# Kernel tuning notes

Hardware: AMD Instinct MI355X
Metric: run time of the kernel (lower is better)

The kernel has to match this reference:

```python
import jax, jax.numpy as jnp
import numpy as np

E, B, D, H, Z = 8, 16384, 512, 512, 64   # experts, batch, input_dim, hidden, latent
NHID = 2                                 # num_mlp_layers - 1 hidden-to-hidden layers


def setup_inputs() -> dict:
    key = jax.random.key(0)
    ks = jax.random.split(key, 12)

    def w(k, shape, fan_in):
        return (jax.random.normal(k, shape, jnp.float32) / np.sqrt(fan_in)).astype(jnp.float32)

    return {
        "x": jax.random.normal(ks[0], (B, D), jnp.float32),
        "eps": jax.random.normal(ks[1], (B, Z), jnp.float32),
        # stacked per-expert parameters (leading axis E)
        "enc_in_w": w(ks[2], (E, D, H), D), "enc_in_b": jnp.zeros((E, H), jnp.float32),
        "enc_hid_w": w(ks[3], (E, NHID, H, H), H), "enc_hid_b": jnp.zeros((E, NHID, H), jnp.float32),
        "mu_w": w(ks[4], (E, H, Z), H), "mu_b": jnp.zeros((E, Z), jnp.float32),
        "lv_w": w(ks[5], (E, H, Z), H), "lv_b": jnp.zeros((E, Z), jnp.float32),
        "dec_in_w": w(ks[6], (E, Z, H), Z), "dec_in_b": jnp.zeros((E, H), jnp.float32),
        "dec_hid_w": w(ks[7], (E, NHID, H, H), H), "dec_hid_b": jnp.zeros((E, NHID, H), jnp.float32),
        "dec_out_w": w(ks[8], (E, H, D), H), "dec_out_b": jnp.zeros((E, D), jnp.float32),
    }


def _moe_forward(x, eps, enc_in_w, enc_in_b, enc_hid_w, enc_hid_b,
                 mu_w, mu_b, lv_w, lv_b,
                 dec_in_w, dec_in_b, dec_hid_w, dec_hid_b, dec_out_w, dec_out_b):
    # ---- every expert tries the problem (dense, all experts over full batch) ----
    h = jax.nn.relu(jnp.einsum('bd,edh->ebh', x, enc_in_w) + enc_in_b[:, None, :])
    for i in range(NHID):
        h = jax.nn.relu(jnp.einsum('ebh,ehk->ebk', h, enc_hid_w[:, i]) + enc_hid_b[:, i, None, :])
    mu = jnp.einsum('ebh,ehz->ebz', h, mu_w) + mu_b[:, None, :]          # [E,B,Z]
    logvar = jnp.einsum('ebh,ehz->ebz', h, lv_w) + lv_b[:, None, :]       # [E,B,Z]
    z = mu + jnp.exp(0.5 * logvar) * eps[None, :, :]                      # reparameterize
    g = jax.nn.relu(jnp.einsum('ebz,ezh->ebh', z, dec_in_w) + dec_in_b[:, None, :])
    for i in range(NHID):
        g = jax.nn.relu(jnp.einsum('ebh,ehk->ebk', g, dec_hid_w[:, i]) + dec_hid_b[:, i, None, :])
    xhat = jnp.einsum('ebh,ehd->ebd', g, dec_out_w) + dec_out_b[:, None, :]  # [E,B,D]

    # ---- per-sample recon loss, pick best expert (torch.min over experts) ----
    recon = jnp.mean((xhat - x[None, :, :]) ** 2, axis=-1)                # [E,B]
    expert_idx = jnp.argmin(recon, axis=0)                                # [B]

    # ---- sparse_others: single fused gather instead of python loop ----
    bi = jnp.arange(x.shape[0])
    return mu[expert_idx, bi], logvar[expert_idx, bi], xhat[expert_idx, bi]


def reference(x, eps, enc_in_w, enc_in_b, enc_hid_w, enc_hid_b,
              mu_w, mu_b, lv_w, lv_b,
              dec_in_w, dec_in_b, dec_hid_w, dec_hid_b, dec_out_w, dec_out_b):
    return _moe_forward(x, eps, enc_in_w, enc_in_b, enc_hid_w, enc_hid_b,
                        mu_w, mu_b, lv_w, lv_b,
                        dec_in_w, dec_in_b, dec_hid_w, dec_hid_b, dec_out_w, dec_out_b)
```

## Files before the change

kernel.cpp:

```cpp
#include <hip/hip_runtime.h>
#include <cstdint>

#define Eexp 8
#define Bb   16384
#define Dd   512
#define Hh   512
#define Zz   64

typedef _Float16 f16x8 __attribute__((ext_vector_type(8)));
typedef float    f32x4 __attribute__((ext_vector_type(4)));

#define OFF_ENCIN  0
#define OFF_HID0   524288
#define OFF_HID1   1048576
#define OFF_HEADS  1572864
#define OFF_DECIN  1703936
#define OFF_DHID0  1769472
#define OFF_DHID1  2293760
#define OFF_DECOUT 2818048
#define PEREXP     3342336
#define WT_TOTAL   (8 * (size_t)PEREXP)
#define FMELEMS    ((size_t)Bb * 512 * 2)
#define ZFME       ((size_t)Bb * 64 * 2)
#define BZE        ((size_t)Bb * 64)

#define GLL16(g, l) __builtin_amdgcn_global_load_lds( \
    (const __attribute__((address_space(1))) void*)(g), \
    (__attribute__((address_space(3))) void*)(l), 16, 0, 0)

template<bool TR>
__global__ __launch_bounds__(256)
void fmsplit(const float* __restrict__ src, _Float16* __restrict__ dst,
             int KTOT, int inner, long sStride, long dStride)
{
    __shared__ float t[64][65];
    const int e  = blockIdx.z;
    const int o0 = blockIdx.x * 64;
    const int k0 = blockIdx.y * 64;
    const float* S = src + (size_t)e * sStride;
    _Float16*    D = dst + (size_t)e * dStride;
    const int tid = threadIdx.x;
    const int rr = tid >> 4, c4 = (tid & 15) * 4;
    #pragma unroll
    for (int p = 0; p < 4; ++p) {
        const int r = rr + p * 16;
        const float4 v = *reinterpret_cast<const float4*>(
            S + (size_t)(TR ? (k0 + r) : (o0 + r)) * inner + (TR ? o0 : k0) + c4);
        t[r][c4 + 0] = v.x; t[r][c4 + 1] = v.y;
        t[r][c4 + 2] = v.z; t[r][c4 + 3] = v.w;
    }
    __syncthreads();
    const int lane = tid & 63, wid = tid >> 6;
    const int KB = KTOT >> 5;
    #pragma unroll
    for (int p = 0; p < 2; ++p) {
        const int g  = wid * 2 + p;
        const int ot = g >> 1, kb = g & 1;
        const int rI = ot * 16 + (lane & 15);
        const int kI = kb * 32 + (lane >> 4) * 8;
        f16x8 hv, lv;
        #pragma unroll
        for (int j = 0; j < 8; ++j) {
            const float v = TR ? t[kI + j][rI] : t[rI][kI + j];
            const _Float16 h = (_Float16)v;
            hv[j] = h; lv[j] = (_Float16)(v - (float)h);
        }
        const size_t base = ((size_t)((o0 >> 4) + ot) * KB + (k0 >> 5) + kb) * 1024;
        *reinterpret_cast<f16x8*>(D + base + lane * 8)       = hv;
        *reinterpret_cast<f16x8*>(D + base + 512 + lane * 8) = lv;
    }
}

template<int KA>
__global__ __launch_bounds__(256, 2)
void gemm_mid(const _Float16* __restrict__ A, const _Float16* __restrict__ W,
              const float* __restrict__ B, _Float16* __restrict__ C)
{
    constexpr int KB  = KA / 32;
    constexpr int NT  = KB;
    constexpr int ACH = 16;
    constexpr int NCH = 32;
    constexpr int GPW = 8;
    __shared__ __align__(16) _Float16 lds[2 * NCH * 512];

    const int bid = blockIdx.x;
    const int bx = (bid & 7) * 16 + (bid >> 5);
    const int by = (bid >> 3) & 3;

    const int lane = threadIdx.x & 63, wid = threadIdx.x >> 6;
    const int wr = wid >> 1, wc = wid & 1;
    const int row0 = bx * 128;
    const int col0 = by * 128;

    const _Float16* src[GPW];
    #pragma unroll
    for (int p = 0; p < GPW; ++p) {
        const int q = wid * GPW + p;
        if (q < ACH)
            src[p] = A + (size_t)((row0 >> 4) + (q >> 1)) * KB * 1024
                       + (q & 1) * 512 + lane * 8;
        else {
            const int qq = q - ACH;
            src[p] = W + (size_t)((col0 >> 4) + (qq >> 1)) * KB * 1024
                       + (qq & 1) * 512 + lane * 8;
        }
    }

    f32x4 acc[4][4];
    #pragma unroll
    for (int i = 0; i < 4; ++i)
        #pragma unroll
        for (int j = 0; j < 4; ++j) acc[i][j] = {0.f, 0.f, 0.f, 0.f};

#define STAGE(buf)                                                           \
    { _Pragma("unroll")                                                      \
      for (int p = 0; p < GPW; ++p) {                                        \
          GLL16(src[p], lds + (buf) * (NCH * 512) + (wid * GPW + p) * 512);  \
          src[p] += 1024;                                                    \
      } }

    STAGE(0)
    if (NT > 1) STAGE(1)

    for (int t = 0; t < NT; ++t) {
        if (t + 1 < NT) { asm volatile("s_waitcnt vmcnt(%0)" :: "i"(GPW) : "memory"); }
        else            { asm volatile("s_waitcnt vmcnt(0)" ::: "memory"); }
        __builtin_amdgcn_s_barrier();
        asm volatile("" ::: "memory");

        const _Float16* B0 = lds + (t & 1) * (NCH * 512);
        f16x8 ah[4], al[4], wh[4], wl[4];
        #pragma unroll
        for (int mf = 0; mf < 4; ++mf) {
            const int q = (wr * 4 + mf) * 2;
            ah[mf] = *reinterpret_cast<const f16x8*>(B0 + q * 512 + lane * 8);
            al[mf] = *reinterpret_cast<const f16x8*>(B0 + q * 512 + 512 + lane * 8);
        }
        #pragma unroll
        for (int nf = 0; nf < 4; ++nf) {
            const int q = ACH + (wc * 4 + nf) * 2;
            wh[nf] = *reinterpret_cast<const f16x8*>(B0 + q * 512 + lane * 8);
            wl[nf] = *reinterpret_cast<const f16x8*>(B0 + q * 512 + 512 + lane * 8);
        }
        __builtin_amdgcn_s_setprio(1);
        #pragma unroll
        for (int mf = 0; mf < 4; ++mf)
            #pragma unroll
            for (int nf = 0; nf < 4; ++nf) {
                acc[mf][nf] = __builtin_amdgcn_mfma_f32_16x16x32_f16(
                    ah[mf], wh[nf], acc[mf][nf], 0, 0, 0);
                acc[mf][nf] = __builtin_amdgcn_mfma_f32_16x16x32_f16(
                    ah[mf], wl[nf], acc[mf][nf], 0, 0, 0);
                acc[mf][nf] = __builtin_amdgcn_mfma_f32_16x16x32_f16(
                    al[mf], wh[nf], acc[mf][nf], 0, 0, 0);
            }
        __builtin_amdgcn_s_setprio(0);
        asm volatile("" ::: "memory");
        __builtin_amdgcn_s_barrier();
        asm volatile("" ::: "memory");
        if (t + 2 < NT) STAGE(t & 1)
    }
#undef STAGE

    uint32_t* sb = reinterpret_cast<uint32_t*>(&lds[0]);
    #pragma unroll
    for (int ph = 0; ph < 2; ++ph) {
        if (wc == ph) {
            #pragma unroll
            for (int nf = 0; nf < 4; ++nf) {
                const int c_l = nf * 16 + (lane & 15);
                const float bv = B[col0 + ph * 64 + c_l];
                #pragma unroll
                for (int mf = 0; mf < 4; ++mf)
                    #pragma unroll
                    for (int j = 0; j < 4; ++j) {
                        const int r_l = wr * 64 + mf * 16 + (lane >> 4) * 4 + j;
                        const float v = fmaxf(acc[mf][nf][j] + bv, 0.f);
                        const _Float16 h = (_Float16)v;
                        const _Float16 lo = (_Float16)(v - (float)h);
                        const uint32_t pk =
                            (uint32_t)__builtin_bit_cast(uint16_t, h) |
                            ((uint32_t)__builtin_bit_cast(uint16_t, lo) << 16);
                        sb[r_l * 64 + (((c_l >> 2) ^ (r_l & 15)) << 2) + (c_l & 3)] = pk;
                    }
            }
        }
        __syncthreads();
        {
            #pragma unroll
            for (int i = 0; i < 4; ++i) {
                const int q = wid * 4 + i;
                const int T_l = q >> 1, kb_l = q & 1;
                const int r_l = T_l * 16 + (lane & 15);
                const int cb  = kb_l * 32 + (lane >> 4) * 8;
                uint32_t u[8];
                #pragma unroll
                for (int jb = 0; jb < 2; ++jb) {
                    const int chunk = ((cb >> 2) + jb) ^ (r_l & 15);
                    const uint32_t* pp = &sb[r_l * 64 + chunk * 4];
                    u[jb*4+0] = pp[0]; u[jb*4+1] = pp[1];
                    u[jb*4+2] = pp[2]; u[jb*4+3] = pp[3];
                }
                f16x8 hv, lvv;
                #pragma unroll
                for (int j = 0; j < 8; ++j) {
                    hv[j]  = __builtin_bit_cast(_Float16, (uint16_t)(u[j] & 0xffff));
                    lvv[j] = __builtin_bit_cast(_Float16, (uint16_t)(u[j] >> 16));
                }
                const size_t base =
                    ((size_t)((row0 >> 4) + T_l) * 16 +
                     ((col0 + ph * 64) >> 5) + kb_l) * 1024;
                *reinterpret_cast<f16x8*>(C + base + lane * 8)       = hv;
                *reinterpret_cast<f16x8*>(C + base + 512 + lane * 8) = lvv;
            }
        }
        __syncthreads();
    }
}

__global__ __launch_bounds__(256, 2)
void heads_z(const _Float16* __restrict__ A, const _Float16* __restrict__ W,
             const float* __restrict__ mu_b, const float* __restrict__ lv_b,
             const float* __restrict__ eps,
             float* __restrict__ mu_e, float* __restrict__ lv_e,
             _Float16* __restrict__ zfm)
{
    constexpr int KB = 16, NT = 16, ACH = 4, NCH = 20, GPW = 5;
    __shared__ __align__(16) _Float16 lds[2 * NCH * 512];

    const int bid = blockIdx.x;
    const int bx = (bid & 7) * 64 + (bid >> 3);
    const int lane = threadIdx.x & 63, wid = threadIdx.x >> 6;
    const int wr = wid >> 1, wc = wid & 1;
    const int row0 = bx * 32;

    const _Float16* src[GPW];
    #pragma unroll
    for (int p = 0; p < GPW; ++p) {
        const int q = wid * GPW + p;
        if (q < ACH)
            src[p] = A + (size_t)((row0 >> 4) + (q >> 1)) * KB * 1024
                       + (q & 1) * 512 + lane * 8;
        else {
            const int qq = q - ACH;
            src[p] = W + (size_t)(qq >> 1) * KB * 1024 + (qq & 1) * 512 + lane * 8;
        }
    }

    f32x4 acc[4];
    #pragma unroll
    for (int j = 0; j < 4; ++j) acc[j] = {0.f, 0.f, 0.f, 0.f};

#define STAGE(buf)                                                           \
    { _Pragma("unroll")                                                      \
      for (int p = 0; p < GPW; ++p) {                                        \
          GLL16(src[p], lds + (buf) * (NCH * 512) + (wid * GPW + p) * 512);  \
          src[p] += 1024;                                                    \
      } }

    STAGE(0)
    STAGE(1)

    for (int t = 0; t < NT; ++t) {
        if (t + 1 < NT) { asm volatile("s_waitcnt vmcnt(%0)" :: "i"(GPW) : "memory"); }
        else            { asm volatile("s_waitcnt vmcnt(0)" ::: "memory"); }
        __builtin_amdgcn_s_barrier();
        asm volatile("" ::: "memory");

        const _Float16* B0 = lds + (t & 1) * (NCH * 512);
        f16x8 ah, al, wh[4], wl[4];
        {
            const int q = wr * 2;
            ah = *reinterpret_cast<const f16x8*>(B0 + q * 512 + lane * 8);
            al = *reinterpret_cast<const f16x8*>(B0 + q * 512 + 512 + lane * 8);
        }
        #pragma unroll
        for (int nf = 0; nf < 4; ++nf) {
            const int q = ACH + (wc * 4 + nf) * 2;
            wh[nf] = *reinterpret_cast<const f16x8*>(B0 + q * 512 + lane * 8);
            wl[nf] = *reinterpret_cast<const f16x8*>(B0 + q * 512 + 512 + lane * 8);
        }
        __builtin_amdgcn_s_setprio(1);
        #pragma unroll
        for (int nf = 0; nf < 4; ++nf) {
            acc[nf] = __builtin_amdgcn_mfma_f32_16x16x32_f16(ah, wh[nf], acc[nf], 0, 0, 0);
            acc[nf] = __builtin_amdgcn_mfma_f32_16x16x32_f16(ah, wl[nf], acc[nf], 0, 0, 0);
            acc[nf] = __builtin_amdgcn_mfma_f32_16x16x32_f16(al, wh[nf], acc[nf], 0, 0, 0);
        }
        __builtin_amdgcn_s_setprio(0);
        asm volatile("" ::: "memory");
        __builtin_amdgcn_s_barrier();
        asm volatile("" ::: "memory");
        if (t + 2 < NT) STAGE(t & 1)
    }
#undef STAGE

    float* mulv = reinterpret_cast<float*>(&lds[0]);
    #pragma unroll
    for (int nf = 0; nf < 4; ++nf) {
        const int c_h = wc * 64 + nf * 16 + (lane & 15);
        const float bv = (c_h < 64) ? mu_b[c_h] : lv_b[c_h - 64];
        #pragma unroll
        for (int j = 0; j < 4; ++j) {
            const int r_l = wr * 16 + (lane >> 4) * 4 + j;
            mulv[r_l * 128 + c_h] = acc[nf][j] + bv;
        }
    }
    __syncthreads();
    const int tid = threadIdx.x;
    #pragma unroll
    for (int k = 0; k < 8; ++k) {
        const int id  = tid + k * 256;
        const int r_l = id >> 6, c = id & 63;
        const float m = mulv[r_l * 128 + c];
        const float l = mulv[r_l * 128 + 64 + c];
        const size_t go = (size_t)(row0 + r_l) * 64 + c;
        const float ev = eps[go];
        const float zv = m + expf(0.5f * l) * ev;
        mu_e[go] = m; lv_e[go] = l;
        const _Float16 h  = (_Float16)zv;
        const _Float16 lo = (_Float16)(zv - (float)h);
        const size_t base = ((size_t)((row0 + r_l) >> 4) * 2 + (c >> 5)) * 1024
                            + ((r_l & 15) + ((c >> 3) & 3) * 16) * 8 + (c & 7);
        zfm[base]       = h;
        zfm[base + 512] = lo;
    }
}

__global__ __launch_bounds__(512, 1)
void dec_out_fused(const _Float16* __restrict__ Afm, const _Float16* __restrict__ Wfm,
                   const float* __restrict__ bias,
                   const float* __restrict__ Xin,
                   const float* __restrict__ mu_e, const float* __restrict__ lv_e,
                   float* __restrict__ best,
                   float* __restrict__ out_mu, float* __restrict__ out_lv,
                   float* __restrict__ out_xh, int isFirst)
{
    constexpr int KB = 16, NT = 16;
    __shared__ __align__(16) _Float16 lds[2 * 8 * 512];

    const int bid = blockIdx.x;
    const int bx = (bid & 7) * 32 + (bid >> 3);
    const int lane = threadIdx.x & 63, wid = threadIdx.x >> 6;
    const int row0 = bx * 64;
    const int colW = wid * 64;

    const _Float16* aSrc = Afm + (size_t)((row0 >> 4) + (wid >> 1)) * KB * 1024
                               + (wid & 1) * 512 + lane * 8;
    const _Float16* wSrc[8];
    #pragma unroll
    for (int i = 0; i < 8; ++i)
        wSrc[i] = Wfm + (size_t)(wid * 4 + (i >> 1)) * KB * 1024
                      + (i & 1) * 512 + lane * 8;

    f32x4 acc[4][4];
    #pragma unroll
    for (int i = 0; i < 4; ++i)
        #pragma unroll
        for (int j = 0; j < 4; ++j) acc[i][j] = {0.f, 0.f, 0.f, 0.f};

#define STAGE_A(buf)                                                         \
    { GLL16(aSrc, lds + (buf) * 4096 + wid * 512); aSrc += 1024; }

    STAGE_A(0)
    STAGE_A(1)

    for (int t = 0; t < NT; ++t) {
        f16x8 wh[4], wl[4];
        #pragma unroll
        for (int nf = 0; nf < 4; ++nf) {
            wh[nf] = *reinterpret_cast<const f16x8*>(wSrc[nf * 2]);
            wl[nf] = *reinterpret_cast<const f16x8*>(wSrc[nf * 2 + 1]);
            wSrc[nf * 2]     += 1024;
            wSrc[nf * 2 + 1] += 1024;
        }
        if (t + 1 < NT) { asm volatile("s_waitcnt vmcnt(9)" ::: "memory"); }
        else            { asm volatile("s_waitcnt vmcnt(8)" ::: "memory"); }
        __builtin_amdgcn_s_barrier();
        asm volatile("" ::: "memory");

        const _Float16* B0 = lds + (t & 1) * 4096;
        f16x8 ah[4], al[4];
        #pragma unroll
        for (int mf = 0; mf < 4; ++mf) {
            ah[mf] = *reinterpret_cast<const f16x8*>(B0 + mf * 1024 + lane * 8);
            al[mf] = *reinterpret_cast<const f16x8*>(B0 + mf * 1024 + 512 + lane * 8);
        }
        __builtin_amdgcn_s_setprio(1);
        #pragma unroll
        for (int mf = 0; mf < 4; ++mf)
            #pragma unroll
            for (int nf = 0; nf < 4; ++nf) {
                acc[mf][nf] = __builtin_amdgcn_mfma_f32_16x16x32_f16(
                    ah[mf], wh[nf], acc[mf][nf], 0, 0, 0);
                acc[mf][nf] = __builtin_amdgcn_mfma_f32_16x16x32_f16(
                    ah[mf], wl[nf], acc[mf][nf], 0, 0, 0);
                acc[mf][nf] = __builtin_amdgcn_mfma_f32_16x16x32_f16(
                    al[mf], wh[nf], acc[mf][nf], 0, 0, 0);
            }
        __builtin_amdgcn_s_setprio(0);
        asm volatile("" ::: "memory");
        __builtin_amdgcn_s_barrier();
        asm volatile("" ::: "memory");
        if (t + 2 < NT) STAGE_A(t & 1)
    }
#undef STAGE_A

    float* recP = reinterpret_cast<float*>(&lds[0]);
    int*   winf = reinterpret_cast<int*>(recP + 8 * 64);

    float rsum[4][4];
    #pragma unroll
    for (int mf = 0; mf < 4; ++mf)
        #pragma unroll
        for (int j = 0; j < 4; ++j) rsum[mf][j] = 0.f;
    float bv[4];
    #pragma unroll
    for (int nf = 0; nf < 4; ++nf) bv[nf] = bias[colW + nf * 16 + (lane & 15)];
    #pragma unroll
    for (int nf = 0; nf < 4; ++nf) {
        const int col = colW + nf * 16 + (lane & 15);
        #pragma unroll
        for (int mf = 0; mf < 4; ++mf)
            #pragma unroll
            for (int j = 0; j < 4; ++j) {
                const int r_l = mf * 16 + (lane >> 4) * 4 + j;
                const float v = acc[mf][nf][j] + bv[nf];
                const float d = v - Xin[(size_t)(row0 + r_l) * 512 + col];
                rsum[mf][j] += d * d;
            }
    }
    #pragma unroll
    for (int mf = 0; mf < 4; ++mf)
        #pragma unroll
        for (int j = 0; j < 4; ++j) {
            float s = rsum[mf][j];
            s += __shfl_xor(s, 1); s += __shfl_xor(s, 2);
            s += __shfl_xor(s, 4); s += __shfl_xor(s, 8);
            if ((lane & 15) == 0)
                recP[wid * 64 + mf * 16 + (lane >> 4) * 4 + j] = s;
        }
    __syncthreads();
    if (wid == 0) {
        float r = 0.f;
        #pragma unroll
        for (int w = 0; w < 8; ++w) r += recP[w * 64 + lane];
        const int grow = row0 + lane;
        const bool w = isFirst || (r < best[grow]);
        if (w) best[grow] = r;
        winf[lane] = w ? 1 : 0;
    }
    __syncthreads();
    #pragma unroll
    for (int mf = 0; mf < 4; ++mf)
        #pragma unroll
        for (int j = 0; j < 4; ++j) {
            const int r_l = mf * 16 + (lane >> 4) * 4 + j;
            if (winf[r_l]) {
                #pragma unroll
                for (int nf = 0; nf < 4; ++nf) {
                    const int col = colW + nf * 16 + (lane & 15);
                    out_xh[(size_t)(row0 + r_l) * 512 + col] = acc[mf][nf][j] + bv[nf];
                }
            }
        }
    #pragma unroll
    for (int k = 0; k < 8; ++k) {
        const int r = wid * 8 + k;
        if (winf[r]) {
            const size_t o = (size_t)(row0 + r) * 64 + lane;
            out_mu[o] = mu_e[o];
            out_lv[o] = lv_e[o];
        }
    }
}

extern "C" void kernel_launch(void* const* d_in, const int* in_sizes, int n_in,
                              void* d_out, int out_size, void* d_ws, size_t ws_size,
                              hipStream_t stream)
{
    const float* x         = (const float*)d_in[0];
    const float* eps       = (const float*)d_in[1];
    const float* enc_in_w  = (const float*)d_in[2];
    const float* enc_in_b  = (const float*)d_in[3];
    const float* enc_hid_w = (const float*)d_in[4];
    const float* enc_hid_b = (const float*)d_in[5];
    const float* mu_w      = (const float*)d_in[6];
    const float* mu_b      = (const float*)d_in[7];
    const float* lv_w      = (const float*)d_in[8];
    const float* lv_b      = (const float*)d_in[9];
    const float* dec_in_w  = (const float*)d_in[10];
    const float* dec_in_b  = (const float*)d_in[11];
    const float* dec_hid_w = (const float*)d_in[12];
    const float* dec_hid_b = (const float*)d_in[13];
    const float* dec_out_w = (const float*)d_in[14];
    const float* dec_out_b = (const float*)d_in[15];

    _Float16* wt  = (_Float16*)d_ws;
    _Float16* xfm = wt + WT_TOTAL;
    _Float16* afm = xfm + FMELEMS;
    _Float16* bfm = afm + FMELEMS;
    _Float16* zfm = bfm + FMELEMS;
    float* fbase  = (float*)(zfm + ZFME);
    float* mu_e   = fbase;
    float* lv_e   = mu_e + BZE;
    float* best   = lv_e + BZE;

    float* out_mu = (float*)d_out;
    float* out_lv = out_mu + (size_t)Bb * Zz;
    float* out_xh = out_lv + (size_t)Bb * Zz;

    const dim3 blk(256);

    fmsplit<true ><<<dim3(8, 8, 8), blk, 0, stream>>>(enc_in_w,           wt + OFF_ENCIN,  512, 512, 262144, PEREXP);
    fmsplit<true ><<<dim3(8, 8, 8), blk, 0, stream>>>(enc_hid_w,          wt + OFF_HID0,   512, 512, 524288, PEREXP);
    fmsplit<true ><<<dim3(8, 8, 8), blk, 0, stream>>>(enc_hid_w + 262144, wt + OFF_HID1,   512, 512, 524288, PEREXP);
    fmsplit<true ><<<dim3(1, 8, 8), blk, 0, stream>>>(mu_w,               wt + OFF_HEADS,  512,  64,  32768, PEREXP);
    fmsplit<true ><<<dim3(1, 8, 8), blk, 0, stream>>>(lv_w,        wt + OFF_HEADS + 65536, 512,  64,  32768, PEREXP);
    fmsplit<true ><<<dim3(8, 1, 8), blk, 0, stream>>>(dec_in_w,           wt + OFF_DECIN,   64, 512,  32768, PEREXP);
    fmsplit<true ><<<dim3(8, 8, 8), blk, 0, stream>>>(dec_hid_w,          wt + OFF_DHID0,  512, 512, 524288, PEREXP);
    fmsplit<true ><<<dim3(8, 8, 8), blk, 0, stream>>>(dec_hid_w + 262144, wt + OFF_DHID1,  512, 512, 524288, PEREXP);
    fmsplit<true ><<<dim3(8, 8, 8), blk, 0, stream>>>(dec_out_w,          wt + OFF_DECOUT, 512, 512, 262144, PEREXP);
    fmsplit<false><<<dim3(256, 8, 1), blk, 0, stream>>>(x,                xfm,             512, 512, 0, 0);

    const dim3 g512(512), g256(256), blk512(512);

    for (int e = 0; e < Eexp; ++e) {
        const _Float16* we = wt + (size_t)e * PEREXP;
        gemm_mid<512><<<g512, blk, 0, stream>>>(
            xfm, we + OFF_ENCIN, enc_in_b + (size_t)e * Hh, afm);
        gemm_mid<512><<<g512, blk, 0, stream>>>(
            afm, we + OFF_HID0, enc_hid_b + ((size_t)e * 2 + 0) * Hh, bfm);
        gemm_mid<512><<<g512, blk, 0, stream>>>(
            bfm, we + OFF_HID1, enc_hid_b + ((size_t)e * 2 + 1) * Hh, afm);
        heads_z<<<g512, blk, 0, stream>>>(
            afm, we + OFF_HEADS, mu_b + (size_t)e * Zz, lv_b + (size_t)e * Zz,
            eps, mu_e, lv_e, zfm);
        gemm_mid< 64><<<g512, blk, 0, stream>>>(
            zfm, we + OFF_DECIN, dec_in_b + (size_t)e * Hh, bfm);
        gemm_mid<512><<<g512, blk, 0, stream>>>(
            bfm, we + OFF_DHID0, dec_hid_b + ((size_t)e * 2 + 0) * Hh, afm);
        gemm_mid<512><<<g512, blk, 0, stream>>>(
            afm, we + OFF_DHID1, dec_hid_b + ((size_t)e * 2 + 1) * Hh, bfm);
        dec_out_fused<<<g256, blk512, 0, stream>>>(
            bfm, we + OFF_DECOUT, dec_out_b + (size_t)e * Dd,
            x, mu_e, lv_e, best, out_mu, out_lv, out_xh, e == 0 ? 1 : 0);
    }
}
```

Before: 1.689 ms.

## Halve dec_out row tile, drop LDS staging, double grid and occupancy

The fused decoder-output kernel now handles 32 rows per block instead of 64 and launches 512 blocks instead of 256, with launch bounds raised to allow two blocks per CU. The LDS double-buffered A staging and its barriers are removed, so each wave loads A fragments straight from global memory. The aim is better CU fill on the 256-CU part and less synchronisation, at the cost of every wave re-reading the same A tile from global/L2 and losing the explicit load/compute overlap.

```diff
diff --git a/kernel.cpp b/kernel.cpp
--- a/kernel.cpp
+++ b/kernel.cpp
@@ -327,7 +327,7 @@
     }
 }
 
-__global__ __launch_bounds__(512, 1)
+__global__ __launch_bounds__(512, 2)
 void dec_out_fused(const _Float16* __restrict__ Afm, const _Float16* __restrict__ Wfm,
                    const float* __restrict__ bias,
                    const float* __restrict__ Xin,
@@ -337,58 +337,50 @@
                    float* __restrict__ out_xh, int isFirst)
 {
     constexpr int KB = 16, NT = 16;
-    __shared__ __align__(16) _Float16 lds[2 * 8 * 512];
+    __shared__ float recP[8 * 32];
+    __shared__ int   winf[32];
 
     const int bid = blockIdx.x;
-    const int bx = (bid & 7) * 32 + (bid >> 3);
+    const int bx = (bid & 7) * 64 + (bid >> 3);
     const int lane = threadIdx.x & 63, wid = threadIdx.x >> 6;
-    const int row0 = bx * 64;
+    const int row0 = bx * 32;
     const int colW = wid * 64;
 
-    const _Float16* aSrc = Afm + (size_t)((row0 >> 4) + (wid >> 1)) * KB * 1024
-                               + (wid & 1) * 512 + lane * 8;
-    const _Float16* wSrc[8];
+    const _Float16* aP[4];
+    #pragma unroll
+    for (int i = 0; i < 4; ++i)
+        aP[i] = Afm + (size_t)((row0 >> 4) + (i >> 1)) * KB * 1024
+                    + (i & 1) * 512 + lane * 8;
+    const _Float16* wP[8];
     #pragma unroll
     for (int i = 0; i < 8; ++i)
-        wSrc[i] = Wfm + (size_t)(wid * 4 + (i >> 1)) * KB * 1024
-                      + (i & 1) * 512 + lane * 8;
-
-    f32x4 acc[4][4];
-    #pragma unroll
-    for (int i = 0; i < 4; ++i)
+        wP[i] = Wfm + (size_t)(wid * 4 + (i >> 1)) * KB * 1024
+                    + (i & 1) * 512 + lane * 8;
+
+    f32x4 acc[2][4];
+    #pragma unroll
+    for (int i = 0; i < 2; ++i)
         #pragma unroll
         for (int j = 0; j < 4; ++j) acc[i][j] = {0.f, 0.f, 0.f, 0.f};
 
-#define STAGE_A(buf)                                                         \
-    { GLL16(aSrc, lds + (buf) * 4096 + wid * 512); aSrc += 1024; }
-
-    STAGE_A(0)
-    STAGE_A(1)
-
     for (int t = 0; t < NT; ++t) {
-        f16x8 wh[4], wl[4];
+        f16x8 ah[2], al[2], wh[4], wl[4];
+        #pragma unroll
+        for (int mf = 0; mf < 2; ++mf) {
+            ah[mf] = *reinterpret_cast<const f16x8*>(aP[mf * 2]);
+            al[mf] = *reinterpret_cast<const f16x8*>(aP[mf * 2 + 1]);
+            aP[mf * 2]     += 1024;
+            aP[mf * 2 + 1] += 1024;
+        }
         #pragma unroll
         for (int nf = 0; nf < 4; ++nf) {
-            wh[nf] = *reinterpret_cast<const f16x8*>(wSrc[nf * 2]);
-            wl[nf] = *reinterpret_cast<const f16x8*>(wSrc[nf * 2 + 1]);
-            wSrc[nf * 2]     += 1024;
-            wSrc[nf * 2 + 1] += 1024;
-        }
-        if (t + 1 < NT) { asm volatile("s_waitcnt vmcnt(9)" ::: "memory"); }
-        else            { asm volatile("s_waitcnt vmcnt(8)" ::: "memory"); }
-        __builtin_amdgcn_s_barrier();
-        asm volatile("" ::: "memory");
-
-        const _Float16* B0 = lds + (t & 1) * 4096;
-        f16x8 ah[4], al[4];
-        #pragma unroll
-        for (int mf = 0; mf < 4; ++mf) {
-            ah[mf] = *reinterpret_cast<const f16x8*>(B0 + mf * 1024 + lane * 8);
-            al[mf] = *reinterpret_cast<const f16x8*>(B0 + mf * 1024 + 512 + lane * 8);
-        }
-        __builtin_amdgcn_s_setprio(1);
-        #pragma unroll
-        for (int mf = 0; mf < 4; ++mf)
+            wh[nf] = *reinterpret_cast<const f16x8*>(wP[nf * 2]);
+            wl[nf] = *reinterpret_cast<const f16x8*>(wP[nf * 2 + 1]);
+            wP[nf * 2]     += 1024;
+            wP[nf * 2 + 1] += 1024;
+        }
+        #pragma unroll
+        for (int mf = 0; mf < 2; ++mf)
             #pragma unroll
             for (int nf = 0; nf < 4; ++nf) {
                 acc[mf][nf] = __builtin_amdgcn_mfma_f32_16x16x32_f16(
@@ -398,20 +390,11 @@
                 acc[mf][nf] = __builtin_amdgcn_mfma_f32_16x16x32_f16(
                     al[mf], wh[nf], acc[mf][nf], 0, 0, 0);
             }
-        __builtin_amdgcn_s_setprio(0);
-        asm volatile("" ::: "memory");
-        __builtin_amdgcn_s_barrier();
-        asm volatile("" ::: "memory");
-        if (t + 2 < NT) STAGE_A(t & 1)
-    }
-#undef STAGE_A
-
-    float* recP = reinterpret_cast<float*>(&lds[0]);
-    int*   winf = reinterpret_cast<int*>(recP + 8 * 64);
-
-    float rsum[4][4];
-    #pragma unroll
-    for (int mf = 0; mf < 4; ++mf)
+    }
+
+    float rsum[2][4];
+    #pragma unroll
+    for (int mf = 0; mf < 2; ++mf)
         #pragma unroll
         for (int j = 0; j < 4; ++j) rsum[mf][j] = 0.f;
     float bv[4];
@@ -421,7 +404,7 @@
     for (int nf = 0; nf < 4; ++nf) {
         const int col = colW + nf * 16 + (lane & 15);
         #pragma unroll
-        for (int mf = 0; mf < 4; ++mf)
+        for (int mf = 0; mf < 2; ++mf)
             #pragma unroll
             for (int j = 0; j < 4; ++j) {
                 const int r_l = mf * 16 + (lane >> 4) * 4 + j;
@@ -431,20 +414,20 @@
             }
     }
     #pragma unroll
-    for (int mf = 0; mf < 4; ++mf)
+    for (int mf = 0; mf < 2; ++mf)
         #pragma unroll
         for (int j = 0; j < 4; ++j) {
             float s = rsum[mf][j];
             s += __shfl_xor(s, 1); s += __shfl_xor(s, 2);
             s += __shfl_xor(s, 4); s += __shfl_xor(s, 8);
             if ((lane & 15) == 0)
-                recP[wid * 64 + mf * 16 + (lane >> 4) * 4 + j] = s;
+                recP[wid * 32 + mf * 16 + (lane >> 4) * 4 + j] = s;
         }
     __syncthreads();
-    if (wid == 0) {
+    if (wid == 0 && lane < 32) {
         float r = 0.f;
         #pragma unroll
-        for (int w = 0; w < 8; ++w) r += recP[w * 64 + lane];
+        for (int w = 0; w < 8; ++w) r += recP[w * 32 + lane];
         const int grow = row0 + lane;
         const bool w = isFirst || (r < best[grow]);
         if (w) best[grow] = r;
@@ -452,7 +435,7 @@
     }
     __syncthreads();
     #pragma unroll
-    for (int mf = 0; mf < 4; ++mf)
+    for (int mf = 0; mf < 2; ++mf)
         #pragma unroll
         for (int j = 0; j < 4; ++j) {
             const int r_l = mf * 16 + (lane >> 4) * 4 + j;
@@ -465,8 +448,8 @@
             }
         }
     #pragma unroll
-    for (int k = 0; k < 8; ++k) {
-        const int r = wid * 8 + k;
+    for (int k = 0; k < 4; ++k) {
+        const int r = wid * 4 + k;
         if (winf[r]) {
             const size_t o = (size_t)(row0 + r) * 64 + lane;
             out_mu[o] = mu_e[o];
@@ -523,7 +506,7 @@
     fmsplit<true ><<<dim3(8, 8, 8), blk, 0, stream>>>(dec_out_w,          wt + OFF_DECOUT, 512, 512, 262144, PEREXP);
     fmsplit<false><<<dim3(256, 8, 1), blk, 0, stream>>>(x,                xfm,             512, 512, 0, 0);
 
-    const dim3 g512(512), g256(256), blk512(512);
+    const dim3 g512(512), blk512(512);
 
     for (int e = 0; e < Eexp; ++e) {
         const _Float16* we = wt + (size_t)e * PEREXP;
@@ -542,7 +525,7 @@
             bfm, we + OFF_DHID0, dec_hid_b + ((size_t)e * 2 + 0) * Hh, afm);
         gemm_mid<512><<<g512, blk, 0, stream>>>(
             afm, we + OFF_DHID1, dec_hid_b + ((size_t)e * 2 + 1) * Hh, bfm);
-        dec_out_fused<<<g256, blk512, 0, stream>>>(
+        dec_out_fused<<<g512, blk512, 0, stream>>>(
             bfm, we + OFF_DECOUT, dec_out_b + (size_t)e * Dd,
             x, mu_e, lv_e, best, out_mu, out_lv, out_xh, e == 0 ? 1 : 0);
     }
```

Result: no change. 1.702 ms (+0.8%).
